# Optimization experiments

Measured on AMD Instinct MI355X. Metric: run time of the kernel, lower is better.

## Reference

```python
import jax, jax.numpy as jnp
import numpy as np

DIM = 192
HEADS = 6
HEAD_DIM = DIM // HEADS          # 32
N_WIN_TOK = 2 * 6 * 12           # 144 tokens per (2,6,12) window
BIAS_ROWS = (2 * 12 - 1) * 6 * 6 * 2 * 2  # 3312
N_WINDOWS = 960


def setup_inputs() -> dict:
    key = jax.random.key(0)
    ks = jax.random.split(key, 8)
    x = jax.random.normal(ks[0], (N_WINDOWS, N_WIN_TOK, DIM), dtype=jnp.float32)
    mask = jax.random.randint(ks[1], (N_WINDOWS, N_WIN_TOK, N_WIN_TOK), 0, 2, dtype=jnp.int32)
    rel_index = jax.random.randint(ks[2], (N_WIN_TOK, N_WIN_TOK), 0, BIAS_ROWS, dtype=jnp.int32)
    # parameters (torch nn.Linear equivalents, stored as [in, out])
    w_qkv = jax.random.normal(ks[3], (DIM, 3 * DIM), dtype=jnp.float32) * 0.02
    b_qkv = jnp.zeros((3 * DIM,), dtype=jnp.float32)
    w_out = jax.random.normal(ks[4], (DIM, DIM), dtype=jnp.float32) * 0.02
    b_out = jnp.zeros((DIM,), dtype=jnp.float32)
    bias_table = jax.random.normal(ks[5], (BIAS_ROWS, HEADS), dtype=jnp.float32) * 0.02
    return {"x": x, "mask": mask, "rel_index": rel_index,
            "w_qkv": w_qkv, "b_qkv": b_qkv, "w_out": w_out, "b_out": b_out,
            "bias_table": bias_table}


def reference(x, mask, rel_index, w_qkv, b_qkv, w_out, b_out, bias_table):
    nW, N, dim = x.shape
    scale = jnp.asarray(HEAD_DIM, x.dtype) ** -0.5
    # qkv projection: [nW, N, 3, heads, head_dim]
    qkv = (x @ w_qkv + b_qkv).reshape(nW, N, 3, HEADS, HEAD_DIM)
    q, k, v = qkv[:, :, 0], qkv[:, :, 1], qkv[:, :, 2]   # each [nW, N, heads, hd]
    # attention scores [nW, heads, N, N]
    attn = jnp.einsum('wnhd,wmhd->whnm', q * scale, k)
    # relative-position bias gather: table[rel_index] -> [N, N, heads] -> [heads, N, N]
    bias = bias_table[rel_index].transpose(2, 0, 1)
    attn = attn + bias[None]
    # additive mask: positions where mask == 0 get -1e9
    attn = jnp.where(mask[:, None, :, :] == 0, jnp.asarray(-1e9, attn.dtype), attn)
    attn = jax.nn.softmax(attn, axis=-1)
    out = jnp.einsum('whnm,wmhd->wnhd', attn, v).reshape(nW, N, dim)
    return out @ w_out + b_out
```

## Files before the change

kernel.cpp:

```cpp
#include <hip/hip_runtime.h>
#include <math.h>

#define NW 960
#define NT 144
#define DIM 192
#define NH 6
#define HD 32
#define WCOLS 576

typedef __bf16 bf16x8 __attribute__((ext_vector_type(8)));
typedef float floatx4 __attribute__((ext_vector_type(4)));

__device__ __forceinline__ unsigned short f2bf(float x) {
    union { float f; unsigned u; } v; v.f = x;
    unsigned r = v.u + 0x7fffu + ((v.u >> 16) & 1u);
    return (unsigned short)(r >> 16);
}
__device__ __forceinline__ float bf2f(unsigned short b) {
    union { unsigned u; float f; } v; v.u = ((unsigned)b) << 16;
    return v.f;
}
__device__ __forceinline__ floatx4 mfma16(bf16x8 a, bf16x8 b, floatx4 c) {
    return __builtin_amdgcn_mfma_f32_16x16x32_bf16(a, b, c, 0, 0, 0);
}
__device__ __forceinline__ bf16x8 lds_ld8(const unsigned short* p) {
    bf16x8 v;
    __builtin_memcpy(&v, p, 16);
    return v;
}

__global__ void prep_bias(const int* __restrict__ rel_index,
                          const float* __restrict__ bias_table,
                          float* __restrict__ bias_pre) {
    int i = blockIdx.x * 256 + threadIdx.x;
    if (i < NH * NT * NT) {
        int h = i / (NT * NT);
        int rem = i - h * (NT * NT);
        bias_pre[i] = bias_table[rel_index[rem] * NH + h];
    }
}

__global__ void prep_wq_frag(const float* __restrict__ w_qkv,
                             unsigned short* __restrict__ wh,
                             unsigned short* __restrict__ wl) {
    int i = blockIdx.x * 256 + threadIdx.x;
    if (i < NH * 6 * 6 * 512) {
        int h = i / 18432; int r = i - h * 18432;
        int j = r / 3072;  r -= j * 3072;
        int kt = r / 512;  r -= kt * 512;
        int lane = r >> 3, pos = r & 7;
        int col96 = j * 16 + (lane & 15);
        int k = kt * 32 + (lane >> 4) * 8 + pos;
        float v = w_qkv[k * WCOLS + (col96 >> 5) * DIM + h * HD + (col96 & 31)];
        unsigned short hi = f2bf(v);
        wh[i] = hi;
        wl[i] = f2bf(v - bf2f(hi));
    }
}

__global__ void prep_wo_frag(const float* __restrict__ w_out,
                             unsigned short* __restrict__ wh,
                             unsigned short* __restrict__ wl) {
    int i = blockIdx.x * 256 + threadIdx.x;
    if (i < 12 * 6 * 512) {
        int nt = i / 3072; int r = i - nt * 3072;
        int kt = r / 512;  r -= kt * 512;
        int lane = r >> 3, pos = r & 7;
        int ocol = nt * 16 + (lane & 15);
        int k = kt * 32 + (lane >> 4) * 8 + pos;
        float v = w_out[k * DIM + ocol];
        unsigned short hi = f2bf(v);
        wh[i] = hi;
        wl[i] = f2bf(v - bf2f(hi));
    }
}

__global__ __launch_bounds__(768, 3)
void fused(const float* __restrict__ x, const int* __restrict__ mask,
           const float* __restrict__ bias_pre,
           const unsigned short* __restrict__ wqh, const unsigned short* __restrict__ wql,
           const float* __restrict__ b_qkv,
           const unsigned short* __restrict__ woh_g, const unsigned short* __restrict__ wol_g,
           const float* __restrict__ b_out, float* __restrict__ out)
{
    __shared__ __align__(16) unsigned short lds[63904];
    const int XFo = 0;
    const int BUF0 = 27648, BUFSZ = 14336;
    const int Q2off = 0, K2off = 4608, V2off = 9216;
    const int Po = 56320, MBo = 62464;

    const int t = threadIdx.x;
    const int w = blockIdx.x;
    const int lane = t & 63, wv = t >> 6;
    const int c = lane & 15, q = lane >> 4;
    const float scale = 0.17677669529663687f;
    const float* xg = x + (size_t)w * NT * DIM;

    {
        unsigned* XFd = (unsigned*)&lds[XFo];
        #pragma unroll
        for (int l = 0; l < 18; ++l) {
            int d = t + l * 768;
            int kt = d / 2304; int r2 = d - kt * 2304;
            int tile = r2 >> 8; int r3 = r2 & 255;
            int ln = r3 >> 2, pp = r3 & 3;
            int n = tile * 16 + (ln & 15);
            int k = kt * 32 + (ln >> 4) * 8 + pp * 2;
            float2 xv = *(const float2*)&xg[n * DIM + k];
            XFd[d] = (unsigned)f2bf(xv.x) | ((unsigned)f2bf(xv.y) << 16);
        }
    }
    for (int e = t; e < 1024; e += 768) {
        int b = e >> 9, r2 = e & 511;
        int gi = r2 >> 8, l2 = 32 + ((r2 >> 3) & 31), pos = r2 & 7;
        lds[BUF0 + b * BUFSZ + V2off + (gi * 5 + 4) * 512 + l2 * 8 + pos] = 0;
    }
    {
        unsigned* mb = (unsigned*)&lds[MBo];
        #pragma unroll 4
        for (int rr = 0; rr < 12; ++rr) {
            int n = wv * 12 + rr;
            const int* mrow = mask + ((size_t)w * NT + n) * NT;
            unsigned long long b0 = __ballot(mrow[lane] != 0);
            unsigned long long b1 = __ballot(mrow[64 + lane] != 0);
            int mv = (lane < 16) ? mrow[128 + lane] : 0;
            unsigned long long b2 = __ballot(mv != 0);
            if (lane == 0) {
                mb[n * 5 + 0] = (unsigned)b0;
                mb[n * 5 + 1] = (unsigned)(b0 >> 32);
                mb[n * 5 + 2] = (unsigned)b1;
                mb[n * 5 + 3] = (unsigned)(b1 >> 32);
                mb[n * 5 + 4] = (unsigned)b2;
            }
        }
    }

    auto qkv_tile = [&](int h, int j, int i3lo, int i3n) {
        const int part = j >> 1, jj = j & 1;
        unsigned short* buf = &lds[BUF0 + (h & 1) * BUFSZ];
        const unsigned short* bhp = wqh + (size_t)((h * 6 + j) * 6) * 512 + lane * 8;
        const unsigned short* blp = wql + (size_t)((h * 6 + j) * 6) * 512 + lane * 8;
        bf16x8 bh[6], bl[6];
        #pragma unroll
        for (int kt = 0; kt < 6; ++kt) {
            bh[kt] = *(const bf16x8*)&bhp[kt * 512];
            bl[kt] = *(const bf16x8*)&blp[kt * 512];
        }
        float bq = b_qkv[part * DIM + h * HD + jj * 16 + c];
        for (int i3x = 0; i3x < i3n; ++i3x) {
            int i3 = i3lo + i3x;
            floatx4 a[3];
            #pragma unroll
            for (int ii = 0; ii < 3; ++ii) a[ii] = (floatx4)0.0f;
            __builtin_amdgcn_s_setprio(1);
            #pragma unroll
            for (int kt = 0; kt < 6; ++kt) {
                #pragma unroll
                for (int ii = 0; ii < 3; ++ii) {
                    bf16x8 ah = *(const bf16x8*)&lds[XFo + (kt * 9 + i3 * 3 + ii) * 512 + lane * 8];
                    a[ii] = mfma16(ah, bh[kt], a[ii]);
                    a[ii] = mfma16(ah, bl[kt], a[ii]);
                }
            }
            __builtin_amdgcn_s_setprio(0);
            #pragma unroll
            for (int ii = 0; ii < 3; ++ii) {
                int i = i3 * 3 + ii;
                #pragma unroll
                for (int r = 0; r < 4; ++r) {
                    float v = a[ii][r] + bq;
                    int col32 = jj * 16 + c;
                    if (part == 0) {
                        buf[Q2off + i * 512 + ((q * 4 + r) + 16 * (col32 >> 3)) * 8 + (col32 & 7)] = f2bf(v * scale);
                    } else if (part == 1) {
                        buf[K2off + i * 512 + ((q * 4 + r) + 16 * (col32 >> 3)) * 8 + (col32 & 7)] = f2bf(v);
                    } else {
                        int n = i * 16 + q * 4 + r;
                        buf[V2off + (jj * 5 + (n >> 5)) * 512 + (c + 16 * ((n >> 3) & 3)) * 8 + (n & 7)] = f2bf(v);
                    }
                }
            }
        }
    };

    auto attn_unit = [&](int h, floatx4 (&O)[2]) {
        const int s = wv;
        unsigned short* buf = &lds[BUF0 + (h & 1) * BUFSZ];
        float bb[4][9];
        const float* bbase = bias_pre + h * (NT * NT) + (s * 16 + q * 4) * NT + c;
        #pragma unroll
        for (int r = 0; r < 4; ++r)
            #pragma unroll
            for (int nt = 0; nt < 9; ++nt)
                bb[r][nt] = bbase[r * NT + nt * 16];
        bf16x8 qf = *(const bf16x8*)&buf[Q2off + s * 512 + lane * 8];
        floatx4 sacc[9];
        __builtin_amdgcn_s_setprio(1);
        #pragma unroll
        for (int nt = 0; nt < 9; ++nt) {
            bf16x8 kf = *(const bf16x8*)&buf[K2off + nt * 512 + lane * 8];
            sacc[nt] = mfma16(qf, kf, (floatx4)0.0f);
        }
        __builtin_amdgcn_s_setprio(0);
        const unsigned* mb = (const unsigned*)&lds[MBo];
        unsigned mwv[4][5];
        #pragma unroll
        for (int r = 0; r < 4; ++r) {
            int n = s * 16 + q * 4 + r;
            #pragma unroll
            for (int k5 = 0; k5 < 5; ++k5) mwv[r][k5] = mb[n * 5 + k5];
        }
        float e[4][9], mx[4];
        #pragma unroll
        for (int r = 0; r < 4; ++r) mx[r] = -1e30f;
        #pragma unroll
        for (int r = 0; r < 4; ++r)
            #pragma unroll
            for (int nt = 0; nt < 9; ++nt) {
                float val = sacc[nt][r] + bb[r][nt];
                unsigned bit = (mwv[r][nt >> 1] >> (((nt & 1) << 4) + c)) & 1u;
                val = bit ? val : -1e9f;
                e[r][nt] = val; mx[r] = fmaxf(mx[r], val);
            }
        #pragma unroll
        for (int o = 8; o; o >>= 1)
            #pragma unroll
            for (int r = 0; r < 4; ++r) mx[r] = fmaxf(mx[r], __shfl_xor(mx[r], o, 64));
        float sum[4] = {0.f, 0.f, 0.f, 0.f};
        #pragma unroll
        for (int r = 0; r < 4; ++r)
            #pragma unroll
            for (int nt = 0; nt < 9; ++nt) { e[r][nt] = __expf(e[r][nt] - mx[r]); sum[r] += e[r][nt]; }
        #pragma unroll
        for (int o = 8; o; o >>= 1)
            #pragma unroll
            for (int r = 0; r < 4; ++r) sum[r] += __shfl_xor(sum[r], o, 64);
        float rinv[4];
        #pragma unroll
        for (int r = 0; r < 4; ++r) rinv[r] = 1.0f / sum[r];
        floatx4 o0 = (floatx4)0.0f, o1 = (floatx4)0.0f;
        unsigned short* pbase = &lds[Po + wv * 512];
        #pragma unroll
        for (int sl = 0; sl < 5; ++sl) {
            asm volatile("" ::: "memory");
            #pragma unroll
            for (int r = 0; r < 4; ++r)
                #pragma unroll
                for (int ntl = 0; ntl < 2; ++ntl) {
                    int nt = 2 * sl + ntl;
                    unsigned short pv = 0;
                    if (nt < 9) pv = f2bf(e[r][nt] * rinv[r]);
                    pbase[((q * 4 + r) + 16 * ((ntl << 1) + (c >> 3))) * 8 + (c & 7)] = pv;
                }
            asm volatile("" ::: "memory");
            bf16x8 pf = lds_ld8(&pbase[lane * 8]);
            __builtin_amdgcn_s_setprio(1);
            o0 = mfma16(pf, *(const bf16x8*)&buf[V2off + (0 * 5 + sl) * 512 + lane * 8], o0);
            o1 = mfma16(pf, *(const bf16x8*)&buf[V2off + (1 * 5 + sl) * 512 + lane * 8], o1);
            __builtin_amdgcn_s_setprio(0);
        }
        O[0] = o0; O[1] = o1;
    };

    floatx4 Oacc[6][2];

    __syncthreads();

    if (wv < 9) qkv_tile(0, wv / 3, wv % 3, 1);
    else        qkv_tile(0, 3 + (wv - 9), 0, 3);

    #pragma unroll
    for (int h = 1; h < 6; ++h) {
        __syncthreads();
        if (wv < 9) {
            attn_unit(h - 1, Oacc[h - 1]);
            qkv_tile(h, wv / 3, wv % 3, 1);
        } else {
            qkv_tile(h, 3 + (wv - 9), 0, 3);
        }
    }

    __syncthreads();
    if (wv < 9) {
        attn_unit(5, Oacc[5]);
        #pragma unroll
        for (int h = 0; h < 6; ++h)
            #pragma unroll
            for (int ntv = 0; ntv < 2; ++ntv)
                #pragma unroll
                for (int r = 0; r < 4; ++r)
                    lds[XFo + (h * 9 + wv) * 512 +
                        ((q * 4 + r) + 16 * (ntv * 2 + (c >> 3))) * 8 + (c & 7)] =
                        f2bf(Oacc[h][ntv][r]);
    }
    __syncthreads();

    {
        const unsigned short* whp = woh_g + (size_t)(wv * 6) * 512 + lane * 8;
        const unsigned short* wlp = wol_g + (size_t)(wv * 6) * 512 + lane * 8;
        bf16x8 wh[6], wlo[6];
        #pragma unroll
        for (int kt = 0; kt < 6; ++kt) {
            wh[kt]  = *(const bf16x8*)&whp[kt * 512];
            wlo[kt] = *(const bf16x8*)&wlp[kt * 512];
        }
        float bo = b_out[wv * 16 + c];
        #pragma unroll
        for (int i3 = 0; i3 < 3; ++i3) {
            floatx4 a2[3];
            #pragma unroll
            for (int ii = 0; ii < 3; ++ii) a2[ii] = (floatx4)0.0f;
            __builtin_amdgcn_s_setprio(1);
            #pragma unroll
            for (int kt = 0; kt < 6; ++kt) {
                #pragma unroll
                for (int ii = 0; ii < 3; ++ii) {
                    bf16x8 af = *(const bf16x8*)&lds[XFo + (kt * 9 + i3 * 3 + ii) * 512 + lane * 8];
                    a2[ii] = mfma16(af, wh[kt], a2[ii]);
                    a2[ii] = mfma16(af, wlo[kt], a2[ii]);
                }
            }
            __builtin_amdgcn_s_setprio(0);
            #pragma unroll
            for (int ii = 0; ii < 3; ++ii) {
                int n0 = (i3 * 3 + ii) * 16 + q * 4;
                #pragma unroll
                for (int r = 0; r < 4; ++r) {
                    size_t ro = ((size_t)w * NT + n0 + r) * DIM;
                    out[ro + wv * 16 + c] = a2[ii][r] + bo;
                }
            }
        }
    }
}

__global__ __launch_bounds__(256, 2)
void attn_kernel(const float* __restrict__ x, const int* __restrict__ mask,
                 const int* __restrict__ rel_index, const float* __restrict__ w_qkv,
                 const float* __restrict__ b_qkv, const float* __restrict__ bias_table,
                 float* __restrict__ out)
{
    __shared__ float smem[19136];
    float* xt = smem;
    float* wt = smem + 4768;
    float* qs = smem;
    float* ks = smem + 4752;
    float* vs = smem + 9504;
    float* S  = smem + 14400;

    const int t  = threadIdx.x;
    const int w  = blockIdx.x / NH;
    const int h  = blockIdx.x % NH;
    const int tx = t & 15;
    const int ty = t >> 4;
    const float scale = 0.17677669529663687f;
    const float* xg = x + (size_t)w * NT * DIM;

    float acc[9][6];
    #pragma unroll
    for (int i = 0; i < 9; ++i)
        #pragma unroll
        for (int j = 0; j < 6; ++j) acc[i][j] = 0.f;

    for (int kt = 0; kt < 6; ++kt) {
        #pragma unroll
        for (int l = 0; l < 18; ++l) {
            int e = t + l * 256;
            int n = e >> 5, kk = e & 31;
            xt[kk * 149 + n] = xg[n * DIM + kt * 32 + kk];
        }
        #pragma unroll
        for (int l = 0; l < 12; ++l) {
            int e = t + l * 256;
            int kk = e / 96, cc = e - kk * 96;
            int col = (cc >> 5) * DIM + h * HD + (cc & 31);
            wt[kk * 96 + cc] = w_qkv[(kt * 32 + kk) * WCOLS + col];
        }
        __syncthreads();
        #pragma unroll
        for (int kk = 0; kk < 32; ++kk) {
            float a[9], b[6];
            #pragma unroll
            for (int i = 0; i < 9; ++i) a[i] = xt[kk * 149 + ty * 9 + i];
            #pragma unroll
            for (int j = 0; j < 6; ++j) b[j] = wt[kk * 96 + tx * 6 + j];
            #pragma unroll
            for (int i = 0; i < 9; ++i)
                #pragma unroll
                for (int j = 0; j < 6; ++j) acc[i][j] = fmaf(a[i], b[j], acc[i][j]);
        }
        __syncthreads();
    }

    #pragma unroll
    for (int j = 0; j < 6; ++j) {
        int cc = tx * 6 + j;
        int part = cc >> 5, jj = cc & 31;
        float bq = b_qkv[part * DIM + h * HD + jj];
        #pragma unroll
        for (int i = 0; i < 9; ++i) {
            int r = ty * 9 + i;
            float val = acc[i][j] + bq;
            if (part == 0)      qs[r * 33 + jj] = val * scale;
            else if (part == 1) ks[r * 33 + jj] = val;
            else                vs[r * 34 + jj] = val;
        }
    }
    __syncthreads();

    const int wave = t >> 6, lane = t & 63;
    for (int rt = 0; rt < 5; ++rt) {
        const int rows = (rt == 4) ? 16 : 32;
        {
            int r0 = ty * 2;
            int n0 = rt * 32 + r0; if (n0 > NT - 1) n0 = NT - 1;
            int n1 = n0 + 1;       if (n1 > NT - 1) n1 = NT - 1;
            int m0 = tx * 9;
            float s0[9], s1[9];
            #pragma unroll
            for (int j = 0; j < 9; ++j) { s0[j] = 0.f; s1[j] = 0.f; }
            #pragma unroll
            for (int kk = 0; kk < 32; ++kk) {
                float a0 = qs[n0 * 33 + kk];
                float a1 = qs[n1 * 33 + kk];
                #pragma unroll
                for (int j = 0; j < 9; ++j) {
                    float bk = ks[(m0 + j) * 33 + kk];
                    s0[j] = fmaf(a0, bk, s0[j]);
                    s1[j] = fmaf(a1, bk, s1[j]);
                }
            }
            if (r0 < rows) {
                #pragma unroll
                for (int j = 0; j < 9; ++j) S[r0 * 148 + m0 + j] = s0[j];
                #pragma unroll
                for (int j = 0; j < 9; ++j) S[(r0 + 1) * 148 + m0 + j] = s1[j];
            }
        }
        __syncthreads();

        for (int r = wave; r < rows; r += 4) {
            int n = rt * 32 + r;
            const int* mrow = mask + ((size_t)w * NT + n) * NT;
            const int* rrow = rel_index + n * NT;
            float e0 = S[r * 148 + lane] + bias_table[rrow[lane] * NH + h];
            if (mrow[lane] == 0) e0 = -1e9f;
            float e1 = S[r * 148 + 64 + lane] + bias_table[rrow[64 + lane] * NH + h];
            if (mrow[64 + lane] == 0) e1 = -1e9f;
            float e2 = -INFINITY;
            if (lane < 16) {
                e2 = S[r * 148 + 128 + lane] + bias_table[rrow[128 + lane] * NH + h];
                if (mrow[128 + lane] == 0) e2 = -1e9f;
            }
            float vmax = fmaxf(fmaxf(e0, e1), e2);
            #pragma unroll
            for (int off = 32; off > 0; off >>= 1)
                vmax = fmaxf(vmax, __shfl_xor(vmax, off, 64));
            float p0 = __expf(e0 - vmax);
            float p1 = __expf(e1 - vmax);
            float p2 = (lane < 16) ? __expf(e2 - vmax) : 0.f;
            float s = p0 + p1 + p2;
            #pragma unroll
            for (int off = 32; off > 0; off >>= 1)
                s += __shfl_xor(s, off, 64);
            float rinv = 1.f / s;
            S[r * 148 + lane] = p0 * rinv;
            S[r * 148 + 64 + lane] = p1 * rinv;
            if (lane < 16) S[r * 148 + 128 + lane] = p2 * rinv;
        }
        __syncthreads();

        {
            int r0 = ty * 2, dd0 = tx * 2;
            if (r0 < rows) {
                float o00 = 0, o01 = 0, o10 = 0, o11 = 0;
                #pragma unroll
                for (int m = 0; m < NT; ++m) {
                    float p0 = S[r0 * 148 + m];
                    float p1 = S[(r0 + 1) * 148 + m];
                    float2 vv = *(const float2*)&vs[m * 34 + dd0];
                    o00 = fmaf(p0, vv.x, o00);
                    o01 = fmaf(p0, vv.y, o01);
                    o10 = fmaf(p1, vv.x, o10);
                    o11 = fmaf(p1, vv.y, o11);
                }
                int n0 = rt * 32 + r0;
                *(float2*)&out[((size_t)(w * NT + n0)) * DIM + h * HD + dd0] = make_float2(o00, o01);
                *(float2*)&out[((size_t)(w * NT + n0 + 1)) * DIM + h * HD + dd0] = make_float2(o10, o11);
            }
        }
        __syncthreads();
    }
}

__global__ __launch_bounds__(256, 2)
void proj_kernel(float* __restrict__ io, const float* __restrict__ w_out,
                 const float* __restrict__ b_out)
{
    __shared__ float in_t[64 * 196];
    __shared__ float wt[32 * 192];
    const int t = threadIdx.x;
    const size_t row0 = (size_t)blockIdx.x * 64;

    #pragma unroll
    for (int l = 0; l < 12; ++l) {
        int e = t + l * 256;
        int r = e / 48, c4 = e - r * 48;
        float4 val = *(const float4*)&io[(row0 + r) * DIM + c4 * 4];
        *(float4*)&in_t[r * 196 + c4 * 4] = val;
    }
    const int tx = t & 15, ty = t >> 4;
    float acc[4][12];
    #pragma unroll
    for (int i = 0; i < 4; ++i)
        #pragma unroll
        for (int j = 0; j < 12; ++j) acc[i][j] = 0.f;

    for (int kt = 0; kt < 6; ++kt) {
        __syncthreads();
        #pragma unroll
        for (int l = 0; l < 6; ++l) {
            int e = t + l * 256;
            int kk = e / 48, c4 = e - kk * 48;
            *(float4*)&wt[kk * 192 + c4 * 4] =
                *(const float4*)&w_out[(kt * 32 + kk) * DIM + c4 * 4];
        }
        __syncthreads();
        #pragma unroll
        for (int kk = 0; kk < 32; ++kk) {
            float a[4];
            #pragma unroll
            for (int i = 0; i < 4; ++i) a[i] = in_t[(ty * 4 + i) * 196 + kt * 32 + kk];
            float b[12];
            #pragma unroll
            for (int j4 = 0; j4 < 3; ++j4) {
                float4 bb = *(const float4*)&wt[kk * 192 + tx * 12 + j4 * 4];
                b[j4 * 4] = bb.x; b[j4 * 4 + 1] = bb.y;
                b[j4 * 4 + 2] = bb.z; b[j4 * 4 + 3] = bb.w;
            }
            #pragma unroll
            for (int i = 0; i < 4; ++i)
                #pragma unroll
                for (int j = 0; j < 12; ++j)
                    acc[i][j] = fmaf(a[i], b[j], acc[i][j]);
        }
    }

    float bo[12];
    #pragma unroll
    for (int j4 = 0; j4 < 3; ++j4) {
        float4 bb = *(const float4*)&b_out[tx * 12 + j4 * 4];
        bo[j4 * 4] = bb.x; bo[j4 * 4 + 1] = bb.y;
        bo[j4 * 4 + 2] = bb.z; bo[j4 * 4 + 3] = bb.w;
    }
    #pragma unroll
    for (int i = 0; i < 4; ++i) {
        size_t r = row0 + ty * 4 + i;
        #pragma unroll
        for (int j4 = 0; j4 < 3; ++j4) {
            float4 o;
            o.x = acc[i][j4 * 4]     + bo[j4 * 4];
            o.y = acc[i][j4 * 4 + 1] + bo[j4 * 4 + 1];
            o.z = acc[i][j4 * 4 + 2] + bo[j4 * 4 + 2];
            o.w = acc[i][j4 * 4 + 3] + bo[j4 * 4 + 3];
            *(float4*)&io[r * DIM + tx * 12 + j4 * 4] = o;
        }
    }
}

extern "C" void kernel_launch(void* const* d_in, const int* in_sizes, int n_in,
                              void* d_out, int out_size, void* d_ws, size_t ws_size,
                              hipStream_t stream) {
    const float* x          = (const float*)d_in[0];
    const int*   mask       = (const int*)d_in[1];
    const int*   rel_index  = (const int*)d_in[2];
    const float* w_qkv      = (const float*)d_in[3];
    const float* b_qkv      = (const float*)d_in[4];
    const float* w_out      = (const float*)d_in[5];
    const float* b_out      = (const float*)d_in[6];
    const float* bias_table = (const float*)d_in[7];
    float* out = (float*)d_out;

    const size_t WS_NEED = 1087488;

    if (ws_size >= WS_NEED) {
        char* ws = (char*)d_ws;
        float*          bias_pre = (float*)ws;
        unsigned short* wq_h     = (unsigned short*)(ws + 497664);
        unsigned short* wq_l     = (unsigned short*)(ws + 718848);
        unsigned short* wo_h     = (unsigned short*)(ws + 940032);
        unsigned short* wo_l     = (unsigned short*)(ws + 1013760);

        hipLaunchKernelGGL(prep_bias, dim3(486), dim3(256), 0, stream,
                           rel_index, bias_table, bias_pre);
        hipLaunchKernelGGL(prep_wq_frag, dim3(432), dim3(256), 0, stream,
                           w_qkv, wq_h, wq_l);
        hipLaunchKernelGGL(prep_wo_frag, dim3(144), dim3(256), 0, stream,
                           w_out, wo_h, wo_l);
        hipLaunchKernelGGL(fused, dim3(NW), dim3(768), 0, stream,
                           x, mask, bias_pre, wq_h, wq_l, b_qkv,
                           wo_h, wo_l, b_out, out);
    } else {
        hipLaunchKernelGGL(attn_kernel, dim3(NW * NH), dim3(256), 0, stream,
                           x, mask, rel_index, w_qkv, b_qkv, bias_table, out);
        hipLaunchKernelGGL(proj_kernel, dim3(NW * NT / 64), dim3(256), 0, stream,
                           out, w_out, b_out);
    }
}
```

Measured before the change: 451.5 us.

## Drop LDS staging of x, shrink fused block to 9 waves for higher occupancy

```diff
diff --git a/kernel.cpp b/kernel.cpp
--- a/kernel.cpp
+++ b/kernel.cpp
@@ -22,6 +22,11 @@
 }
 __device__ __forceinline__ floatx4 mfma16(bf16x8 a, bf16x8 b, floatx4 c) {
     return __builtin_amdgcn_mfma_f32_16x16x32_bf16(a, b, c, 0, 0, 0);
+}
+__device__ __forceinline__ unsigned cvt_pk(float lo, float hi) {
+    unsigned r;
+    asm("v_cvt_pk_bf16_f32 %0, %1, %2" : "=v"(r) : "v"(lo), "v"(hi));
+    return r;
 }
 __device__ __forceinline__ bf16x8 lds_ld8(const unsigned short* p) {
     bf16x8 v;
@@ -75,7 +80,7 @@
     }
 }
 
-__global__ __launch_bounds__(768, 3)
+__global__ __launch_bounds__(576, 5)
 void fused(const float* __restrict__ x, const int* __restrict__ mask,
            const float* __restrict__ bias_pre,
            const unsigned short* __restrict__ wqh, const unsigned short* __restrict__ wql,
@@ -83,11 +88,11 @@
            const unsigned short* __restrict__ woh_g, const unsigned short* __restrict__ wol_g,
            const float* __restrict__ b_out, float* __restrict__ out)
 {
-    __shared__ __align__(16) unsigned short lds[63904];
-    const int XFo = 0;
-    const int BUF0 = 27648, BUFSZ = 14336;
+    __shared__ __align__(16) unsigned short lds[34720];
+    const int BUF0 = 0, BUFSZ = 14336;
     const int Q2off = 0, K2off = 4608, V2off = 9216;
-    const int Po = 56320, MBo = 62464;
+    const int Po = 28672, MBo = 33280;
+    const int Oo = 0;
 
     const int t = threadIdx.x;
     const int w = blockIdx.x;
@@ -96,21 +101,7 @@
     const float scale = 0.17677669529663687f;
     const float* xg = x + (size_t)w * NT * DIM;
 
-    {
-        unsigned* XFd = (unsigned*)&lds[XFo];
-        #pragma unroll
-        for (int l = 0; l < 18; ++l) {
-            int d = t + l * 768;
-            int kt = d / 2304; int r2 = d - kt * 2304;
-            int tile = r2 >> 8; int r3 = r2 & 255;
-            int ln = r3 >> 2, pp = r3 & 3;
-            int n = tile * 16 + (ln & 15);
-            int k = kt * 32 + (ln >> 4) * 8 + pp * 2;
-            float2 xv = *(const float2*)&xg[n * DIM + k];
-            XFd[d] = (unsigned)f2bf(xv.x) | ((unsigned)f2bf(xv.y) << 16);
-        }
-    }
-    for (int e = t; e < 1024; e += 768) {
+    for (int e = t; e < 1024; e += 576) {
         int b = e >> 9, r2 = e & 511;
         int gi = r2 >> 8, l2 = 32 + ((r2 >> 3) & 31), pos = r2 & 7;
         lds[BUF0 + b * BUFSZ + V2off + (gi * 5 + 4) * 512 + l2 * 8 + pos] = 0;
@@ -118,8 +109,8 @@
     {
         unsigned* mb = (unsigned*)&lds[MBo];
         #pragma unroll 4
-        for (int rr = 0; rr < 12; ++rr) {
-            int n = wv * 12 + rr;
+        for (int rr = 0; rr < 16; ++rr) {
+            int n = wv * 16 + rr;
             const int* mrow = mask + ((size_t)w * NT + n) * NT;
             unsigned long long b0 = __ballot(mrow[lane] != 0);
             unsigned long long b1 = __ballot(mrow[64 + lane] != 0);
@@ -135,49 +126,51 @@
         }
     }
 
-    auto qkv_tile = [&](int h, int j, int i3lo, int i3n) {
+    auto qkv_job = [&](int h, int job) {
+        const int j = job / 3, i3 = job % 3;
         const int part = j >> 1, jj = j & 1;
         unsigned short* buf = &lds[BUF0 + (h & 1) * BUFSZ];
         const unsigned short* bhp = wqh + (size_t)((h * 6 + j) * 6) * 512 + lane * 8;
         const unsigned short* blp = wql + (size_t)((h * 6 + j) * 6) * 512 + lane * 8;
-        bf16x8 bh[6], bl[6];
+        const float* abase = xg + (size_t)(i3 * 48 + (lane & 15)) * DIM + (lane >> 4) * 8;
+        float bq = b_qkv[part * DIM + h * HD + jj * 16 + c];
+        floatx4 a[3];
+        #pragma unroll
+        for (int ii = 0; ii < 3; ++ii) a[ii] = (floatx4)0.0f;
+        __builtin_amdgcn_s_setprio(1);
         #pragma unroll
         for (int kt = 0; kt < 6; ++kt) {
-            bh[kt] = *(const bf16x8*)&bhp[kt * 512];
-            bl[kt] = *(const bf16x8*)&blp[kt * 512];
-        }
-        float bq = b_qkv[part * DIM + h * HD + jj * 16 + c];
-        for (int i3x = 0; i3x < i3n; ++i3x) {
-            int i3 = i3lo + i3x;
-            floatx4 a[3];
-            #pragma unroll
-            for (int ii = 0; ii < 3; ++ii) a[ii] = (floatx4)0.0f;
-            __builtin_amdgcn_s_setprio(1);
-            #pragma unroll
-            for (int kt = 0; kt < 6; ++kt) {
-                #pragma unroll
-                for (int ii = 0; ii < 3; ++ii) {
-                    bf16x8 ah = *(const bf16x8*)&lds[XFo + (kt * 9 + i3 * 3 + ii) * 512 + lane * 8];
-                    a[ii] = mfma16(ah, bh[kt], a[ii]);
-                    a[ii] = mfma16(ah, bl[kt], a[ii]);
-                }
-            }
-            __builtin_amdgcn_s_setprio(0);
+            bf16x8 bh = *(const bf16x8*)&bhp[kt * 512];
+            bf16x8 bl = *(const bf16x8*)&blp[kt * 512];
             #pragma unroll
             for (int ii = 0; ii < 3; ++ii) {
-                int i = i3 * 3 + ii;
-                #pragma unroll
-                for (int r = 0; r < 4; ++r) {
-                    float v = a[ii][r] + bq;
-                    int col32 = jj * 16 + c;
-                    if (part == 0) {
-                        buf[Q2off + i * 512 + ((q * 4 + r) + 16 * (col32 >> 3)) * 8 + (col32 & 7)] = f2bf(v * scale);
-                    } else if (part == 1) {
-                        buf[K2off + i * 512 + ((q * 4 + r) + 16 * (col32 >> 3)) * 8 + (col32 & 7)] = f2bf(v);
-                    } else {
-                        int n = i * 16 + q * 4 + r;
-                        buf[V2off + (jj * 5 + (n >> 5)) * 512 + (c + 16 * ((n >> 3) & 3)) * 8 + (n & 7)] = f2bf(v);
-                    }
+                const float* ap = abase + (size_t)ii * 16 * DIM + kt * 32;
+                float4 v0 = *(const float4*)ap;
+                float4 v1 = *(const float4*)(ap + 4);
+                union { unsigned u[4]; bf16x8 v; } A;
+                A.u[0] = cvt_pk(v0.x, v0.y);
+                A.u[1] = cvt_pk(v0.z, v0.w);
+                A.u[2] = cvt_pk(v1.x, v1.y);
+                A.u[3] = cvt_pk(v1.z, v1.w);
+                a[ii] = mfma16(A.v, bh, a[ii]);
+                a[ii] = mfma16(A.v, bl, a[ii]);
+            }
+        }
+        __builtin_amdgcn_s_setprio(0);
+        #pragma unroll
+        for (int ii = 0; ii < 3; ++ii) {
+            int i = i3 * 3 + ii;
+            #pragma unroll
+            for (int r = 0; r < 4; ++r) {
+                float v = a[ii][r] + bq;
+                int col32 = jj * 16 + c;
+                if (part == 0) {
+                    buf[Q2off + i * 512 + ((q * 4 + r) + 16 * (col32 >> 3)) * 8 + (col32 & 7)] = f2bf(v * scale);
+                } else if (part == 1) {
+                    buf[K2off + i * 512 + ((q * 4 + r) + 16 * (col32 >> 3)) * 8 + (col32 & 7)] = f2bf(v);
+                } else {
+                    int n = i * 16 + q * 4 + r;
+                    buf[V2off + (jj * 5 + (n >> 5)) * 512 + (c + 16 * ((n >> 3) & 3)) * 8 + (n & 7)] = f2bf(v);
                 }
             }
         }
@@ -262,51 +255,18 @@
         O[0] = o0; O[1] = o1;
     };
 
-    floatx4 Oacc[6][2];
-
-    __syncthreads();
-
-    if (wv < 9) qkv_tile(0, wv / 3, wv % 3, 1);
-    else        qkv_tile(0, 3 + (wv - 9), 0, 3);
-
-    #pragma unroll
-    for (int h = 1; h < 6; ++h) {
-        __syncthreads();
-        if (wv < 9) {
-            attn_unit(h - 1, Oacc[h - 1]);
-            qkv_tile(h, wv / 3, wv % 3, 1);
-        } else {
-            qkv_tile(h, 3 + (wv - 9), 0, 3);
-        }
-    }
-
-    __syncthreads();
-    if (wv < 9) {
-        attn_unit(5, Oacc[5]);
-        #pragma unroll
-        for (int h = 0; h < 6; ++h)
-            #pragma unroll
-            for (int ntv = 0; ntv < 2; ++ntv)
-                #pragma unroll
-                for (int r = 0; r < 4; ++r)
-                    lds[XFo + (h * 9 + wv) * 512 +
-                        ((q * 4 + r) + 16 * (ntv * 2 + (c >> 3))) * 8 + (c & 7)] =
-                        f2bf(Oacc[h][ntv][r]);
-    }
-    __syncthreads();
-
-    {
-        const unsigned short* whp = woh_g + (size_t)(wv * 6) * 512 + lane * 8;
-        const unsigned short* wlp = wol_g + (size_t)(wv * 6) * 512 + lane * 8;
+    auto outproj_tile = [&](int colt, int i3lo, int i3n) {
+        const unsigned short* whp = woh_g + (size_t)(colt * 6) * 512 + lane * 8;
+        const unsigned short* wlp = wol_g + (size_t)(colt * 6) * 512 + lane * 8;
         bf16x8 wh[6], wlo[6];
         #pragma unroll
         for (int kt = 0; kt < 6; ++kt) {
             wh[kt]  = *(const bf16x8*)&whp[kt * 512];
             wlo[kt] = *(const bf16x8*)&wlp[kt * 512];
         }
-        float bo = b_out[wv * 16 + c];
-        #pragma unroll
-        for (int i3 = 0; i3 < 3; ++i3) {
+        float bo = b_out[colt * 16 + c];
+        for (int i3x = 0; i3x < i3n; ++i3x) {
+            int i3 = i3lo + i3x;
             floatx4 a2[3];
             #pragma unroll
             for (int ii = 0; ii < 3; ++ii) a2[ii] = (floatx4)0.0f;
@@ -315,7 +275,7 @@
             for (int kt = 0; kt < 6; ++kt) {
                 #pragma unroll
                 for (int ii = 0; ii < 3; ++ii) {
-                    bf16x8 af = *(const bf16x8*)&lds[XFo + (kt * 9 + i3 * 3 + ii) * 512 + lane * 8];
+                    bf16x8 af = *(const bf16x8*)&lds[Oo + (kt * 9 + i3 * 3 + ii) * 512 + lane * 8];
                     a2[ii] = mfma16(af, wh[kt], a2[ii]);
                     a2[ii] = mfma16(af, wlo[kt], a2[ii]);
                 }
@@ -327,11 +287,42 @@
                 #pragma unroll
                 for (int r = 0; r < 4; ++r) {
                     size_t ro = ((size_t)w * NT + n0 + r) * DIM;
-                    out[ro + wv * 16 + c] = a2[ii][r] + bo;
+                    out[ro + colt * 16 + c] = a2[ii][r] + bo;
                 }
             }
         }
-    }
+    };
+
+    floatx4 Oacc[6][2];
+
+    __syncthreads();
+
+    qkv_job(0, wv); qkv_job(0, wv + 9);
+
+    #pragma unroll
+    for (int h = 1; h < 6; ++h) {
+        __syncthreads();
+        attn_unit(h - 1, Oacc[h - 1]);
+        qkv_job(h, wv); qkv_job(h, wv + 9);
+    }
+
+    __syncthreads();
+    attn_unit(5, Oacc[5]);
+
+    __syncthreads();
+    #pragma unroll
+    for (int h = 0; h < 6; ++h)
+        #pragma unroll
+        for (int ntv = 0; ntv < 2; ++ntv)
+            #pragma unroll
+            for (int r = 0; r < 4; ++r)
+                lds[Oo + (h * 9 + wv) * 512 +
+                    ((q * 4 + r) + 16 * (ntv * 2 + (c >> 3))) * 8 + (c & 7)] =
+                    f2bf(Oacc[h][ntv][r]);
+    __syncthreads();
+
+    outproj_tile(wv, 0, 3);
+    outproj_tile(9 + wv / 3, wv % 3, 1);
 }
 
 __global__ __launch_bounds__(256, 2)
@@ -597,7 +588,7 @@
                            w_qkv, wq_h, wq_l);
         hipLaunchKernelGGL(prep_wo_frag, dim3(144), dim3(256), 0, stream,
                            w_out, wo_h, wo_l);
-        hipLaunchKernelGGL(fused, dim3(NW), dim3(768), 0, stream,
+        hipLaunchKernelGGL(fused, dim3(NW), dim3(576), 0, stream,
                            x, mask, bias_pre, wq_h, wq_l, b_qkv,
                            wo_h, wo_l, b_out, out);
     } else {
```

Measured after the change: 1.184 ms. +162.2%, slower.
